# Optimization experiments

Measured on AMD Instinct MI355X. Metric: run time of the kernel, lower is better.

Reference implementation:

```python
import jax, jax.numpy as jnp
import numpy as np

HID = 512
FSI = int(HID * 0.3)            # 153
ALM_EXC = HID - FSI             # 359
ALM_INHIB = FSI                 # 153
UNITS = HID * 6 + FSI           # 3225
HALF = HID // 2
INP_DIM = 1
OUT_DIM = 1
B, T = 64, 500
T_CONST = 0.1
SIG_R = 0.01
SIG_I = 0.01
ALM_OFF = 5 * HID + FSI


def _ht(w):
    # F.hardtanh(w, 1e-10, 1): Dale's-law positivity clamp on raw weights
    return jnp.clip(w, 1e-10, 1.0)


def _build_W(str2str_w, thal2alm_w, thal2str_w, alm2alm_w, alm2str_w, alm2thal_w,
             str2snr_w, str2gpe_w, gpe2stn_w, stn2snr_w, snr2thal_w,
             fsi2str_w, thal2fsi_w, alm2fsi_w, fsi2fsi_w, sparse_mask):
    sm = sparse_mask.astype(str2str_w.dtype)
    alm_sign = jnp.concatenate([jnp.ones(ALM_EXC), -jnp.ones(ALM_INHIB)])      # alm2alm_D diag
    alm_exc_col = jnp.concatenate([jnp.ones(ALM_EXC), jnp.zeros(ALM_INHIB)])   # alm2{str,thal,fsi}_mask
    d1_col = jnp.concatenate([jnp.ones(HALF), jnp.zeros(HALF)])                # D1 half of striatum
    blocks = {
        ('str', 'str'): -(sm * _ht(str2str_w)),                      # @ str2str_D (-I)
        ('str', 'fsi'): -_ht(fsi2str_w),                             # @ fsi2str_D (-I)
        ('str', 'thal'): _ht(thal2str_w) * d1_col[:, None],          # thal2str_mask (D1 rows)
        ('str', 'alm'): _ht(alm2str_w) * alm_exc_col[None, :],
        ('fsi', 'fsi'): -_ht(fsi2fsi_w),                             # @ fsi2fsi_D (-I)
        ('fsi', 'thal'): _ht(thal2fsi_w),
        ('fsi', 'alm'): _ht(alm2fsi_w) * alm_exc_col[None, :],
        ('gpe', 'str'): -(_ht(str2gpe_w) * (1.0 - d1_col)[None, :]), # D2 cols, @ -I
        ('stn', 'gpe'): -_ht(gpe2stn_w),                             # @ gpe2stn_D (-I)
        ('snr', 'str'): -(_ht(str2snr_w) * d1_col[None, :]),         # D1 cols, @ -I
        ('snr', 'stn'): _ht(stn2snr_w),
        ('thal', 'snr'): -_ht(snr2thal_w),                           # @ snr2thal_D (-I)
        ('thal', 'alm'): _ht(alm2thal_w) * alm_exc_col[None, :],
        ('alm', 'thal'): _ht(thal2alm_w),
        ('alm', 'alm'): _ht(alm2alm_w) * alm_sign[None, :],          # @ alm2alm_D
    }
    off = {'str': 0, 'fsi': HID, 'gpe': HID + FSI, 'stn': 2 * HID + FSI,
           'snr': 3 * HID + FSI, 'thal': 4 * HID + FSI, 'alm': 5 * HID + FSI}
    W = jnp.zeros((UNITS, UNITS), str2str_w.dtype)
    for (dst, src), M in blocks.items():
        W = W.at[off[dst]:off[dst] + M.shape[0], off[src]:off[src] + M.shape[1]].set(M)
    return W


def _tonic_and_masks():
    # order: str | fsi | gpe | stn | snr | thal | alm_exc | alm_inhib
    tonic = jnp.concatenate([0.1 * jnp.ones(HID), 0.1 * jnp.ones(FSI),
                             0.6 * jnp.ones(HID), 0.3 * jnp.ones(HID),
                             0.6 * jnp.ones(HID), 0.1 * jnp.ones(HID),
                             0.1 * jnp.ones(ALM_EXC), 0.1 * jnp.ones(ALM_INHIB)])
    thal_mask = jnp.zeros(UNITS).at[4 * HID + FSI:5 * HID + FSI].set(1.0)
    return tonic, thal_mask


def _forward(inp, cue_inp, inhib_stim, hn, xn, noise_hid, noise_inp,
             str2str_w, thal2alm_w, thal2str_w, alm2alm_w, alm2str_w, alm2thal_w,
             str2snr_w, str2gpe_w, gpe2stn_w, stn2snr_w, snr2thal_w,
             fsi2str_w, thal2fsi_w, alm2fsi_w, fsi2fsi_w, inp_w, out_w, sparse_mask):
    W = _build_W(str2str_w, thal2alm_w, thal2str_w, alm2alm_w, alm2str_w, alm2thal_w,
                 str2snr_w, str2gpe_w, gpe2stn_w, stn2snr_w, snr2thal_w,
                 fsi2str_w, thal2fsi_w, alm2fsi_w, fsi2fsi_w, sparse_mask)
    tonic, thal_mask = _tonic_and_masks()
    # input only projects to str+fsi block
    inp_full_w = jnp.concatenate([inp_w, jnp.zeros((5 * HID, inp_w.shape[1]), inp_w.dtype)], axis=0)
    nh_scale = SIG_R * float(np.sqrt(2.0 * T_CONST))
    ni_scale = SIG_I * float(np.sqrt(2.0 * T_CONST))
    x0, h0 = xn[0], hn[0]

    def step(carry, xs):
        x, h = carry
        inp_t, cue_t, inhib_t, nh_t, ni_t = xs
        inp_eff = inp_t + ni_scale * ni_t                               # [B, inp_dim]
        drive = (h @ W.T + inp_eff @ inp_full_w.T
                 + cue_t * thal_mask[None, :] + tonic[None, :]
                 + inhib_t + nh_scale * nh_t)                           # [B, UNITS]
        x_new = x + T_CONST * (-x + drive)
        h_new = jax.nn.relu(x_new)
        out = h_new[:, ALM_OFF:ALM_OFF + ALM_EXC] @ out_w.T             # [B, out_dim]
        return (x_new, h_new), (h_new, out)

    seqs = (jnp.swapaxes(inp, 0, 1), jnp.swapaxes(cue_inp, 0, 1),
            jnp.swapaxes(inhib_stim, 0, 1), noise_hid, noise_inp)
    _, (hs, outs) = jax.lax.scan(step, (x0, h0), seqs)
    return jnp.swapaxes(hs, 0, 1), jnp.swapaxes(outs, 0, 1)


def setup_inputs():
    key = jax.random.key(0)
    ks = jax.random.split(key, 24)
    u = lambda k, shape: jax.random.uniform(k, shape, jnp.float32, 0.0, 0.01)
    return dict(
        inp=jax.random.uniform(ks[0], (B, T, INP_DIM)),
        cue_inp=jax.random.uniform(ks[1], (B, T, 1)),
        inhib_stim=jnp.zeros((B, T, UNITS)),
        hn=jnp.zeros((1, B, UNITS)),
        xn=jnp.zeros((1, B, UNITS)),
        noise_hid=jax.random.normal(ks[2], (T, B, UNITS)),
        noise_inp=jax.random.normal(ks[3], (T, B, INP_DIM)),
        str2str_w=u(ks[4], (HID, HID)),
        thal2alm_w=u(ks[5], (HID, HID)),
        thal2str_w=u(ks[6], (HID, HID)),
        alm2alm_w=u(ks[7], (HID, HID)),
        alm2str_w=u(ks[8], (HID, HID)),
        alm2thal_w=u(ks[9], (HID, HID)),
        str2snr_w=u(ks[10], (HID, HID)),
        str2gpe_w=u(ks[11], (HID, HID)),
        gpe2stn_w=u(ks[12], (HID, HID)),
        stn2snr_w=u(ks[13], (HID, HID)),
        snr2thal_w=u(ks[14], (HID, HID)),
        fsi2str_w=u(ks[15], (HID, FSI)),
        thal2fsi_w=u(ks[16], (FSI, HID)),
        alm2fsi_w=u(ks[17], (FSI, HID)),
        fsi2fsi_w=u(ks[18], (FSI, FSI)),
        inp_w=u(ks[19], (HID + FSI, INP_DIM)),
        out_w=u(ks[20], (OUT_DIM, ALM_EXC)),
        str2str_sparse_mask=(jax.random.uniform(ks[21], (HID, HID)) < 0.1).astype(jnp.int32),
    )


def reference(inp, cue_inp, inhib_stim, hn, xn, noise_hid, noise_inp,
              str2str_w, thal2alm_w, thal2str_w, alm2alm_w, alm2str_w, alm2thal_w,
              str2snr_w, str2gpe_w, gpe2stn_w, stn2snr_w, snr2thal_w,
              fsi2str_w, thal2fsi_w, alm2fsi_w, fsi2fsi_w, inp_w, out_w,
              str2str_sparse_mask):
    return _forward(inp, cue_inp, inhib_stim, hn, xn, noise_hid, noise_inp,
                    str2str_w, thal2alm_w, thal2str_w, alm2alm_w, alm2str_w, alm2thal_w,
                    str2snr_w, str2gpe_w, gpe2stn_w, stn2snr_w, snr2thal_w,
                    fsi2str_w, thal2fsi_w, alm2fsi_w, fsi2fsi_w, inp_w, out_w,
                    str2str_sparse_mask)
```

## Files before the change

### kernel.cpp

```cpp
#include <hip/hip_runtime.h>
#include <hip/hip_cooperative_groups.h>

namespace cg = cooperative_groups;

#define UNITS 3225
#define HSTR  3232
#define NBATCH 64
#define NSTEP 500
#define NH_SCALE 0.004472135954999579f
#define NI_SCALE 0.004472135954999579f
#define HSZ 103200000ll
#define WCT_FLOATS 2731520
#define WC0_FLOATS 2699776
#define NBLK5 125
#define NTHR5 512

__constant__ int   c_dst[7]  = {0,512,665,1177,1689,2201,2713};
__constant__ int   c_rows[7] = {512,153,512,512,512,512,512};
__constant__ int   c_wid[7]  = {1536,1024,256,512,768,871,1024};
__constant__ int   c_r0s[7]  = {0,512,256,665,0,1689,2201};
__constant__ int   c_r0l[7]  = {665,153,256,512,256,512,1024};
__constant__ int   c_r1s[7]  = {2201,2201,0,0,1177,2713,0};
__constant__ float c_ton[7]  = {0.1f,0.1f,0.6f,0.3f,0.6f,0.1f,0.1f};

__constant__ int   c5_rpb[7]  = {16,24,32,32,32,32,24};
__constant__ int   c5_cs[8]   = {0,32,39,55,71,87,103,125};
__constant__ int   c5_wb[8]   = {0,786432,958464,1089536,1351680,1744896,2190848,2731520};
__constant__ int   c5_pdst[7] = {0,512,668,1180,1692,2204,2716};
__constant__ int   c5_pr0s[7] = {0,512,256,668,0,1692,2204};
__constant__ int   c5_pr1s[7] = {2204,2204,0,0,1180,2716,2716};

__constant__ int   c0_cs[8]   = {0,64,84,148,212,276,340,404};
__constant__ int   c0_base[7] = {0,786432,943104,1074176,1336320,1729536,2175488};
__constant__ int   c0_cbase[8]= {0,786432,943104,1074176,1336320,1729536,2175488,2699776};

__device__ __forceinline__ float ht_clip(float w) {
    return fminf(fmaxf(w, 1e-10f), 1.0f);
}

__device__ __forceinline__ float w_val(
    int r, int i, int c,
    const float* __restrict__ str2str, const float* __restrict__ thal2alm,
    const float* __restrict__ thal2str, const float* __restrict__ alm2alm,
    const float* __restrict__ alm2str, const float* __restrict__ alm2thal,
    const float* __restrict__ str2snr, const float* __restrict__ str2gpe,
    const float* __restrict__ gpe2stn, const float* __restrict__ stn2snr,
    const float* __restrict__ snr2thal, const float* __restrict__ fsi2str,
    const float* __restrict__ thal2fsi, const float* __restrict__ alm2fsi,
    const float* __restrict__ fsi2fsi, const int* __restrict__ smask)
{
    int r0l = c_r0l[r];
    int v = (c < r0l) ? (c_r0s[r] + c) : (c_r1s[r] + (c - r0l));
    int rv, j;
    if (v < 512)       { rv = 0; j = v; }
    else if (v < 665)  { rv = 1; j = v - 512; }
    else if (v < 1177) { rv = 2; j = v - 665; }
    else if (v < 1689) { rv = 3; j = v - 1177; }
    else if (v < 2201) { rv = 4; j = v - 1689; }
    else if (v < 2713) { rv = 5; j = v - 2201; }
    else               { rv = 6; j = v - 2713; }
    float val = 0.0f;
    switch (r) {
    case 0:
        if (rv == 0)      val = smask[i*512+j] ? -ht_clip(str2str[i*512+j]) : 0.0f;
        else if (rv == 1) val = -ht_clip(fsi2str[i*153+j]);
        else if (rv == 5) val = (i < 256) ? ht_clip(thal2str[i*512+j]) : 0.0f;
        else              val = (j < 359) ? ht_clip(alm2str[i*512+j]) : 0.0f;
        break;
    case 1:
        if (rv == 1)      val = -ht_clip(fsi2fsi[i*153+j]);
        else if (rv == 5) val = ht_clip(thal2fsi[i*512+j]);
        else              val = (j < 359) ? ht_clip(alm2fsi[i*512+j]) : 0.0f;
        break;
    case 2:
        val = (j >= 256) ? -ht_clip(str2gpe[i*512+j]) : 0.0f;
        break;
    case 3:
        val = -ht_clip(gpe2stn[i*512+j]);
        break;
    case 4:
        if (rv == 0) val = (j < 256) ? -ht_clip(str2snr[i*512+j]) : 0.0f;
        else         val = ht_clip(stn2snr[i*512+j]);
        break;
    case 5:
        if (rv == 4) val = -ht_clip(snr2thal[i*512+j]);
        else         val = (j < 359) ? ht_clip(alm2thal[i*512+j]) : 0.0f;
        break;
    default:
        if (rv == 5) val = ht_clip(thal2alm[i*512+j]);
        else         val = (j < 359) ? ht_clip(alm2alm[i*512+j]) : -ht_clip(alm2alm[i*512+j]);
        break;
    }
    return val;
}

#define WARGS                                                                  \
    const float* __restrict__ str2str, const float* __restrict__ thal2alm,     \
    const float* __restrict__ thal2str, const float* __restrict__ alm2alm,     \
    const float* __restrict__ alm2str, const float* __restrict__ alm2thal,     \
    const float* __restrict__ str2snr, const float* __restrict__ str2gpe,      \
    const float* __restrict__ gpe2stn, const float* __restrict__ stn2snr,      \
    const float* __restrict__ snr2thal, const float* __restrict__ fsi2str,     \
    const float* __restrict__ thal2fsi, const float* __restrict__ alm2fsi,     \
    const float* __restrict__ fsi2fsi, const int* __restrict__ smask
#define WPASS str2str, thal2alm, thal2str, alm2alm, alm2str, alm2thal,         \
    str2snr, str2gpe, gpe2stn, stn2snr, snr2thal, fsi2str, thal2fsi, alm2fsi,  \
    fsi2fsi, smask

__global__ void build_w_v5(WARGS, float* __restrict__ Wct)
{
    int tid = blockIdx.x * blockDim.x + threadIdx.x;
    if (tid >= WCT_FLOATS) return;
    int r = 0;
    while (tid >= c5_wb[r+1]) ++r;
    int local = tid - c5_wb[r];
    int rpb   = c5_rpb[r];
    int width = c_wid[r];
    int bsz   = width * rpb;
    int blk   = local / bsz;
    int rem   = local - blk*bsz;
    int c     = rem / rpb;
    int q     = rem - c*rpb;
    int i     = blk*rpb + q;
    float val = 0.0f;
    if (i < c_rows[r]) val = w_val(r, i, c, WPASS);
    Wct[tid] = val;
}

__global__ void build_w_r0(WARGS, float* __restrict__ Wc)
{
    int tid = blockIdx.x * blockDim.x + threadIdx.x;
    if (tid >= WC0_FLOATS) return;
    int r = 0;
    while (tid >= c0_cbase[r+1]) ++r;
    int local = tid - c0_cbase[r];
    int width = c_wid[r];
    int row = local / width;
    int c = local - row * width;
    Wc[tid] = w_val(r, row, c, WPASS);
}

struct Params {
    const float* __restrict__ inp;
    const float* __restrict__ cue;
    const float* __restrict__ inhib;
    const float* __restrict__ hn;
    const float* __restrict__ xn;
    const float* __restrict__ noise_hid;
    const float* __restrict__ noise_inp;
    const float* __restrict__ inp_w;
    const float* __restrict__ out_w;
    const float* __restrict__ Wc;
    float* __restrict__ hT0;
    float* __restrict__ hT1;
    float* __restrict__ out;
};

template<int RPB, int HALF>
__device__ __forceinline__ void mm_seg(
    const float* __restrict__ rbb,
    const float* __restrict__ wq,
    int cfrom, int cto, int abase,
    float* __restrict__ acc)
{
    int c = cfrom;
    while (c < cto && ((abase + c) & 3)) {
        float hv = rbb[abase + c];
        #pragma unroll
        for (int q = 0; q < HALF; ++q) acc[q] += wq[c*RPB + q] * hv;
        ++c;
    }
    #pragma unroll 2
    for (; c + 4 <= cto; c += 4) {
        const float4 h4 = *reinterpret_cast<const float4*>(&rbb[abase + c]);
        const float hvv[4] = {h4.x, h4.y, h4.z, h4.w};
        #pragma unroll
        for (int cc = 0; cc < 4; ++cc) {
            #pragma unroll
            for (int g = 0; g < HALF/4; ++g) {
                const float4 w4 = *reinterpret_cast<const float4*>(&wq[(c+cc)*RPB + 4*g]);
                acc[4*g+0] += w4.x * hvv[cc];
                acc[4*g+1] += w4.y * hvv[cc];
                acc[4*g+2] += w4.z * hvv[cc];
                acc[4*g+3] += w4.w * hvv[cc];
            }
        }
    }
    for (; c < cto; ++c) {
        float hv = rbb[abase + c];
        #pragma unroll
        for (int q = 0; q < HALF; ++q) acc[q] += wq[c*RPB + q] * hv;
    }
}

template<int RPB, int HALF>
__device__ __forceinline__ void mm_do(
    const float* __restrict__ rbb, const float* __restrict__ wq,
    int c0, int a1, int b0, int c1, int pr0s, int pr1s, int r0l,
    float* __restrict__ red, int kq, int q0, int lane)
{
    float acc[HALF];
    #pragma unroll
    for (int q = 0; q < HALF; ++q) acc[q] = 0.0f;
    mm_seg<RPB,HALF>(rbb, wq, c0, a1, pr0s, acc);
    mm_seg<RPB,HALF>(rbb, wq, b0, c1, pr1s - r0l, acc);
    #pragma unroll
    for (int q = 0; q < HALF; ++q)
        red[(kq*32 + q0 + q)*64 + lane] = acc[q];
}

__global__ void __launch_bounds__(NTHR5, 1) rnn_loop_v5(Params p)
{
    cg::grid_group grid = cg::this_grid();
    const int tid  = threadIdx.x;
    const int lane = tid & 63;
    const int wv   = tid >> 6;
    const int kq   = __builtin_amdgcn_readfirstlane(wv & 3);
    const int grp  = __builtin_amdgcn_readfirstlane(wv >> 2);
    const int bi   = blockIdx.x;

    int r = 0;
    while (bi >= c5_cs[r+1]) ++r;
    const int lc    = bi - c5_cs[r];
    const int rpb   = c5_rpb[r];
    const int row0  = lc * rpb;
    const int nr    = min(rpb, c_rows[r] - row0);
    const int u0    = c_dst[r] + row0;
    const int u0p   = c5_pdst[r] + row0;
    const int width = c_wid[r];
    const float tonic = c_ton[r];
    const int r0l = c_r0l[r];
    const int pr0s = c5_pr0s[r], pr1s = c5_pr1s[r];
    const float* __restrict__ wblk = p.Wc + c5_wb[r] + lc * width * rpb;

    __shared__ float red[4*32*64];
    __shared__ float htile[32*65];

    const int r2 = wv;
    const int b  = lane;

    float xreg[4] = {0.f,0.f,0.f,0.f};
    #pragma unroll
    for (int pi = 0; pi < 4; ++pi) {
        int pr = r2 + 8*pi;
        if (pr < nr) {
            int u = u0 + pr;
            xreg[pi] = p.xn[b*UNITS + u];
            p.hT0[b*HSTR + u0p + pr] = p.hn[b*UNITS + u];
        }
    }
    if (bi == 0) {
        for (int idx = tid; idx < 64*7; idx += NTHR5) {
            int bb2 = idx / 7, k = idx - bb2*7;
            int col = (k < 3) ? (665 + k) : (3225 + k);
            p.hT0[bb2*HSTR + col] = 0.0f;
            p.hT1[bb2*HSTR + col] = 0.0f;
        }
    }
    const bool outs_block = (bi >= 39 && bi < 103);
    const int  ob = bi - 39;
    grid.sync();

    const int c0 = __builtin_amdgcn_readfirstlane((width * kq) >> 2);
    const int c1 = __builtin_amdgcn_readfirstlane((width * (kq + 1)) >> 2);
    const int q0 = __builtin_amdgcn_readfirstlane(grp * (rpb >> 1));
    const int a1 = min(c1, r0l), b0 = max(c0, r0l);
    const float* __restrict__ wq = wblk + q0;

    for (int t = 0; t < NSTEP; ++t) {
        const float* __restrict__ rb = (t & 1) ? p.hT1 : p.hT0;
        float* __restrict__ wb = (t & 1) ? p.hT0 : p.hT1;

        if (outs_block && t > 0 && tid < 64) {
            float s = 0.0f;
            for (int jj = lane; jj < 359; jj += 64)
                s += rb[ob*HSTR + 2716 + jj] * p.out_w[jj];
            #pragma unroll
            for (int off = 32; off > 0; off >>= 1)
                s += __shfl_down(s, off, 64);
            if (lane == 0) p.out[HSZ + (long long)ob*NSTEP + (t-1)] = s;
        }

        float nh[4] = {0.f,0.f,0.f,0.f}, ih[4] = {0.f,0.f,0.f,0.f};
        #pragma unroll
        for (int pi = 0; pi < 4; ++pi) {
            int pr = r2 + 8*pi;
            if (pr < nr) {
                int u = u0 + pr;
                nh[pi] = __builtin_nontemporal_load(&p.noise_hid[((long long)t*NBATCH + b)*UNITS + u]);
                ih[pi] = __builtin_nontemporal_load(&p.inhib[((long long)b*NSTEP + t)*UNITS + u]);
            }
        }
        const float inp_eff = p.inp[b*NSTEP + t] + NI_SCALE * p.noise_inp[t*NBATCH + b];
        const float cue_b   = p.cue[b*NSTEP + t];

        const float* __restrict__ rbb = rb + lane*HSTR;
        if (r == 0)
            mm_do<16,8 >(rbb, wq, c0, a1, b0, c1, pr0s, pr1s, r0l, red, kq, q0, lane);
        else if (r == 1 || r == 6)
            mm_do<24,12>(rbb, wq, c0, a1, b0, c1, pr0s, pr1s, r0l, red, kq, q0, lane);
        else
            mm_do<32,16>(rbb, wq, c0, a1, b0, c1, pr0s, pr1s, r0l, red, kq, q0, lane);
        __syncthreads();

        #pragma unroll
        for (int pi = 0; pi < 4; ++pi) {
            int pr = r2 + 8*pi;
            if (pr < nr) {
                int u = u0 + pr;
                float mm = red[(0*32 + pr)*64 + b];
                mm += red[(1*32 + pr)*64 + b];
                mm += red[(2*32 + pr)*64 + b];
                mm += red[(3*32 + pr)*64 + b];
                float drive = mm + tonic;
                if (u < 665) drive += inp_eff * p.inp_w[u];
                if (u >= 2201 && u < 2713) drive += cue_b;
                drive += ih[pi];
                drive += NH_SCALE * nh[pi];
                float xv = xreg[pi];
                xv = xv + 0.1f*(drive - xv);
                xreg[pi] = xv;
                float h = fmaxf(xv, 0.0f);
                wb[b*HSTR + u0p + pr] = h;
                htile[pr*65 + b] = h;
            }
        }
        __syncthreads();
        {
            int rr = tid & 31, bb = tid >> 5;
            if (rr < nr) {
                #pragma unroll
                for (int rep = 0; rep < 4; ++rep) {
                    int bbb = bb + 16*rep;
                    long long o = (long long)bbb*(NSTEP*UNITS) + (long long)t*UNITS + (u0+rr);
                    __builtin_nontemporal_store(htile[rr*65 + bbb], &p.out[o]);
                }
            }
        }
        grid.sync();
    }

    if (outs_block && tid < 64) {
        const float* __restrict__ rb = p.hT0;
        float s = 0.0f;
        for (int jj = lane; jj < 359; jj += 64)
            s += rb[ob*HSTR + 2716 + jj] * p.out_w[jj];
        #pragma unroll
        for (int off = 32; off > 0; off >>= 1)
            s += __shfl_down(s, off, 64);
        if (lane == 0) p.out[HSZ + (long long)ob*NSTEP + (NSTEP-1)] = s;
    }
}

__global__ void __launch_bounds__(256) rnn_loop_fb(Params p)
{
    cg::grid_group grid = cg::this_grid();
    const int tid  = threadIdx.x;
    const int lane = tid & 63;
    const int wv   = tid >> 6;
    const int bi   = blockIdx.x;

    int r = 0;
    while (bi >= c0_cs[r+1]) ++r;
    const int lc    = bi - c0_cs[r];
    const int row0  = lc * 8;
    const int nr    = min(8, c_rows[r] - row0);
    const int u0    = c_dst[r] + row0;
    const int width = c_wid[r];
    const float tonic = c_ton[r];
    const int r0s = c_r0s[r], r0l = c_r0l[r], r1s = c_r1s[r];
    const float* __restrict__ wr = p.Wc + c0_base[r] + row0 * width;

    __shared__ float red[4][8][64];
    __shared__ float htile[8*65];

    const int r2 = tid >> 6;
    const int b  = tid & 63;

    float xreg[2];
    #pragma unroll
    for (int pi = 0; pi < 2; ++pi) {
        int pr = r2 + 4*pi;
        xreg[pi] = 0.0f;
        if (pr < nr) {
            xreg[pi] = p.xn[b*UNITS + (u0+pr)];
            p.hT0[(u0+pr)*64 + b] = p.hn[b*UNITS + (u0+pr)];
        }
    }
    const bool outs_block = (bi >= 84 && bi < 148);
    grid.sync();

    const int c0 = (width * wv) >> 2;
    const int c1 = (width * (wv+1)) >> 2;
    const int a0 = c0, a1 = min(c1, r0l);
    const int b0 = max(c0, r0l), b1 = c1;

    for (int t = 0; t < NSTEP; ++t) {
        const float* __restrict__ rb = (t & 1) ? p.hT1 : p.hT0;
        float* __restrict__ wb = (t & 1) ? p.hT0 : p.hT1;

        if (outs_block && t > 0 && tid < 64) {
            int ob = bi - 84;
            float s = 0.0f;
            for (int jj = lane; jj < 359; jj += 64)
                s += rb[(2713+jj)*64 + ob] * p.out_w[jj];
            #pragma unroll
            for (int off = 32; off > 0; off >>= 1)
                s += __shfl_down(s, off, 64);
            if (lane == 0) p.out[HSZ + (long long)ob*NSTEP + (t-1)] = s;
        }

        float acc[8];
        #pragma unroll
        for (int q = 0; q < 8; ++q) acc[q] = 0.0f;

        #pragma unroll 4
        for (int c = a0; c < a1; ++c) {
            float hv = rb[(r0s + c)*64 + lane];
            #pragma unroll
            for (int q = 0; q < 8; ++q) acc[q] += wr[q*width + c] * hv;
        }
        #pragma unroll 4
        for (int c = b0; c < b1; ++c) {
            float hv = rb[(r1s + (c - r0l))*64 + lane];
            #pragma unroll
            for (int q = 0; q < 8; ++q) acc[q] += wr[q*width + c] * hv;
        }

        #pragma unroll
        for (int q = 0; q < 8; ++q) red[wv][q][lane] = acc[q];
        __syncthreads();

        const float inp_eff = p.inp[b*NSTEP + t] + NI_SCALE * p.noise_inp[t*NBATCH + b];
        const float cue_b   = p.cue[b*NSTEP + t];
        #pragma unroll
        for (int pi = 0; pi < 2; ++pi) {
            int pr = r2 + 4*pi;
            if (pr < nr) {
                int u = u0 + pr;
                float mm = red[0][pr][b] + red[1][pr][b] + red[2][pr][b] + red[3][pr][b];
                float drive = mm + tonic;
                if (u < 665) drive += inp_eff * p.inp_w[u];
                if (u >= 2201 && u < 2713) drive += cue_b;
                drive += p.inhib[((long long)b*NSTEP + t)*UNITS + u];
                drive += NH_SCALE * p.noise_hid[((long long)t*NBATCH + b)*UNITS + u];
                float xv = xreg[pi];
                xv = xv + 0.1f*(drive - xv);
                xreg[pi] = xv;
                float h = fmaxf(xv, 0.0f);
                wb[u*64 + b] = h;
                htile[pr*65 + b] = h;
            }
        }
        __syncthreads();
        {
            int rr = tid & 7, bb = tid >> 3;
            if (rr < nr) {
                long long o = (long long)bb*(NSTEP*UNITS) + (long long)t*UNITS + (u0+rr);
                p.out[o] = htile[rr*65 + bb];
                p.out[o + 32ll*NSTEP*UNITS] = htile[rr*65 + bb + 32];
            }
        }
        grid.sync();
    }

    if (outs_block && tid < 64) {
        int ob = bi - 84;
        const float* __restrict__ rb = p.hT0;
        float s = 0.0f;
        for (int jj = lane; jj < 359; jj += 64)
            s += rb[(2713+jj)*64 + ob] * p.out_w[jj];
        #pragma unroll
        for (int off = 32; off > 0; off >>= 1)
            s += __shfl_down(s, off, 64);
        if (lane == 0) p.out[HSZ + (long long)ob*NSTEP + (NSTEP-1)] = s;
    }
}

extern "C" void kernel_launch(void* const* d_in, const int* in_sizes, int n_in,
                              void* d_out, int out_size, void* d_ws, size_t ws_size,
                              hipStream_t stream)
{
    (void)in_sizes; (void)n_in; (void)out_size; (void)ws_size;
    const float* inp       = (const float*)d_in[0];
    const float* cue       = (const float*)d_in[1];
    const float* inhib     = (const float*)d_in[2];
    const float* hn        = (const float*)d_in[3];
    const float* xn        = (const float*)d_in[4];
    const float* noise_hid = (const float*)d_in[5];
    const float* noise_inp = (const float*)d_in[6];
    const float* str2str   = (const float*)d_in[7];
    const float* thal2alm  = (const float*)d_in[8];
    const float* thal2str  = (const float*)d_in[9];
    const float* alm2alm   = (const float*)d_in[10];
    const float* alm2str   = (const float*)d_in[11];
    const float* alm2thal  = (const float*)d_in[12];
    const float* str2snr   = (const float*)d_in[13];
    const float* str2gpe   = (const float*)d_in[14];
    const float* gpe2stn   = (const float*)d_in[15];
    const float* stn2snr   = (const float*)d_in[16];
    const float* snr2thal  = (const float*)d_in[17];
    const float* fsi2str   = (const float*)d_in[18];
    const float* thal2fsi  = (const float*)d_in[19];
    const float* alm2fsi   = (const float*)d_in[20];
    const float* fsi2fsi   = (const float*)d_in[21];
    const float* inp_w     = (const float*)d_in[22];
    const float* out_w     = (const float*)d_in[23];
    const int*   smask     = (const int*)d_in[24];

    float* Wct = (float*)d_ws;
    float* hT0 = Wct + WCT_FLOATS;
    float* hT1 = hT0 + NBATCH*HSTR;

    Params p;
    p.inp = inp; p.cue = cue; p.inhib = inhib; p.hn = hn; p.xn = xn;
    p.noise_hid = noise_hid; p.noise_inp = noise_inp;
    p.inp_w = inp_w; p.out_w = out_w; p.Wc = Wct;
    p.hT0 = hT0; p.hT1 = hT1; p.out = (float*)d_out;

    hipLaunchKernelGGL(build_w_v5, dim3((WCT_FLOATS+255)/256), dim3(256), 0, stream,
        str2str, thal2alm, thal2str, alm2alm, alm2str, alm2thal, str2snr, str2gpe,
        gpe2stn, stn2snr, snr2thal, fsi2str, thal2fsi, alm2fsi, fsi2fsi, smask, Wct);

    void* kargs[] = { &p };
    hipError_t ce = hipLaunchCooperativeKernel((void*)rnn_loop_v5,
                                               dim3(NBLK5), dim3(NTHR5), kargs, 0, stream);
    if (ce != hipSuccess) {
        (void)hipGetLastError();
        hipLaunchKernelGGL(build_w_r0, dim3((WC0_FLOATS+255)/256), dim3(256), 0, stream,
            str2str, thal2alm, thal2str, alm2alm, alm2str, alm2thal, str2snr, str2gpe,
            gpe2stn, stn2snr, snr2thal, fsi2str, thal2fsi, alm2fsi, fsi2fsi, smask, Wct);
        hipLaunchCooperativeKernel((void*)rnn_loop_fb,
                                   dim3(404), dim3(256), kargs, 0, stream);
    }
}
```

Before: 41.87 ms.

## Replace grid.sync with atomic counter barrier and transpose hidden-state layout

Swaps the cooperative-groups grid sync for a hand-written monotonic atomic counter barrier, reset by the weight-build kernel, which spins with s_sleep. The hidden-state buffers are transposed to unit-major [unit][batch] so each lane reads its batch value with a coalesced agent-scope atomic load, replacing the padded float4 row reads. The goal is to cut per-step barrier latency over 500 steps. The trade-off is scalar (non-vectorised) h loads, and the fallback path still uses the old layout assumptions.

```diff
diff --git a/kernel.cpp b/kernel.cpp
--- a/kernel.cpp
+++ b/kernel.cpp
@@ -4,7 +4,6 @@
 namespace cg = cooperative_groups;
 
 #define UNITS 3225
-#define HSTR  3232
 #define NBATCH 64
 #define NSTEP 500
 #define NH_SCALE 0.004472135954999579f
@@ -12,8 +11,8 @@
 #define HSZ 103200000ll
 #define WCT_FLOATS 2731520
 #define WC0_FLOATS 2699776
-#define NBLK5 125
-#define NTHR5 512
+#define NBLK6 125
+#define NTHR6 512
 
 __constant__ int   c_dst[7]  = {0,512,665,1177,1689,2201,2713};
 __constant__ int   c_rows[7] = {512,153,512,512,512,512,512};
@@ -23,12 +22,9 @@
 __constant__ int   c_r1s[7]  = {2201,2201,0,0,1177,2713,0};
 __constant__ float c_ton[7]  = {0.1f,0.1f,0.6f,0.3f,0.6f,0.1f,0.1f};
 
-__constant__ int   c5_rpb[7]  = {16,24,32,32,32,32,24};
-__constant__ int   c5_cs[8]   = {0,32,39,55,71,87,103,125};
-__constant__ int   c5_wb[8]   = {0,786432,958464,1089536,1351680,1744896,2190848,2731520};
-__constant__ int   c5_pdst[7] = {0,512,668,1180,1692,2204,2716};
-__constant__ int   c5_pr0s[7] = {0,512,256,668,0,1692,2204};
-__constant__ int   c5_pr1s[7] = {2204,2204,0,0,1180,2716,2716};
+__constant__ int   c6_rpb[7]  = {16,24,32,32,32,32,24};
+__constant__ int   c6_cs[8]   = {0,32,39,55,71,87,103,125};
+__constant__ int   c6_wb[8]   = {0,786432,958464,1089536,1351680,1744896,2190848,2731520};
 
 __constant__ int   c0_cs[8]   = {0,64,84,148,212,276,340,404};
 __constant__ int   c0_base[7] = {0,786432,943104,1074176,1336320,1729536,2175488};
@@ -36,6 +32,13 @@
 
 __device__ __forceinline__ float ht_clip(float w) {
     return fminf(fmaxf(w, 1e-10f), 1.0f);
+}
+
+__device__ __forceinline__ float agload(const float* pp) {
+    return __hip_atomic_load(pp, __ATOMIC_RELAXED, __HIP_MEMORY_SCOPE_AGENT);
+}
+__device__ __forceinline__ void agstore(float* pp, float v) {
+    __hip_atomic_store(pp, v, __ATOMIC_RELAXED, __HIP_MEMORY_SCOPE_AGENT);
 }
 
 __device__ __forceinline__ float w_val(
@@ -107,14 +110,15 @@
     str2snr, str2gpe, gpe2stn, stn2snr, snr2thal, fsi2str, thal2fsi, alm2fsi,  \
     fsi2fsi, smask
 
-__global__ void build_w_v5(WARGS, float* __restrict__ Wct)
+__global__ void build_w_v6(WARGS, float* __restrict__ Wct, unsigned* __restrict__ cnt)
 {
     int tid = blockIdx.x * blockDim.x + threadIdx.x;
+    if (tid == 0) { cnt[0] = 0u; }
     if (tid >= WCT_FLOATS) return;
     int r = 0;
-    while (tid >= c5_wb[r+1]) ++r;
-    int local = tid - c5_wb[r];
-    int rpb   = c5_rpb[r];
+    while (tid >= c6_wb[r+1]) ++r;
+    int local = tid - c6_wb[r];
+    int rpb   = c6_rpb[r];
     int width = c_wid[r];
     int bsz   = width * rpb;
     int blk   = local / bsz;
@@ -153,65 +157,64 @@
     const float* __restrict__ Wc;
     float* __restrict__ hT0;
     float* __restrict__ hT1;
+    unsigned* __restrict__ cnt;
     float* __restrict__ out;
 };
 
-template<int RPB, int HALF>
-__device__ __forceinline__ void mm_seg(
-    const float* __restrict__ rbb,
-    const float* __restrict__ wq,
-    int cfrom, int cto, int abase,
-    float* __restrict__ acc)
-{
-    int c = cfrom;
-    while (c < cto && ((abase + c) & 3)) {
-        float hv = rbb[abase + c];
-        #pragma unroll
-        for (int q = 0; q < HALF; ++q) acc[q] += wq[c*RPB + q] * hv;
-        ++c;
-    }
-    #pragma unroll 2
-    for (; c + 4 <= cto; c += 4) {
-        const float4 h4 = *reinterpret_cast<const float4*>(&rbb[abase + c]);
-        const float hvv[4] = {h4.x, h4.y, h4.z, h4.w};
-        #pragma unroll
-        for (int cc = 0; cc < 4; ++cc) {
-            #pragma unroll
-            for (int g = 0; g < HALF/4; ++g) {
-                const float4 w4 = *reinterpret_cast<const float4*>(&wq[(c+cc)*RPB + 4*g]);
-                acc[4*g+0] += w4.x * hvv[cc];
-                acc[4*g+1] += w4.y * hvv[cc];
-                acc[4*g+2] += w4.z * hvv[cc];
-                acc[4*g+3] += w4.w * hvv[cc];
-            }
-        }
-    }
-    for (; c < cto; ++c) {
-        float hv = rbb[abase + c];
-        #pragma unroll
-        for (int q = 0; q < HALF; ++q) acc[q] += wq[c*RPB + q] * hv;
-    }
+__device__ __forceinline__ void gbarrier(unsigned* cnt, unsigned target)
+{
+    asm volatile("s_waitcnt vmcnt(0)" ::: "memory");
+    __syncthreads();
+    if (threadIdx.x == 0) {
+        __hip_atomic_fetch_add(cnt, 1u, __ATOMIC_RELAXED, __HIP_MEMORY_SCOPE_AGENT);
+        while (__hip_atomic_load(cnt, __ATOMIC_RELAXED, __HIP_MEMORY_SCOPE_AGENT) < target)
+            __builtin_amdgcn_s_sleep(2);
+    }
+    __syncthreads();
+    asm volatile("" ::: "memory");
 }
 
 template<int RPB, int HALF>
 __device__ __forceinline__ void mm_do(
-    const float* __restrict__ rbb, const float* __restrict__ wq,
-    int c0, int a1, int b0, int c1, int pr0s, int pr1s, int r0l,
+    const float* __restrict__ rb, const float* __restrict__ wq,
+    int c0, int a1, int b0, int c1, int r0s, int r1s, int r0l,
     float* __restrict__ red, int kq, int q0, int lane)
 {
     float acc[HALF];
     #pragma unroll
     for (int q = 0; q < HALF; ++q) acc[q] = 0.0f;
-    mm_seg<RPB,HALF>(rbb, wq, c0, a1, pr0s, acc);
-    mm_seg<RPB,HALF>(rbb, wq, b0, c1, pr1s - r0l, acc);
+
+    #pragma unroll 4
+    for (int c = c0; c < a1; ++c) {
+        float hv = agload(&rb[(r0s + c)*64 + lane]);
+        #pragma unroll
+        for (int g = 0; g < HALF/4; ++g) {
+            const float4 w4 = *reinterpret_cast<const float4*>(&wq[c*RPB + 4*g]);
+            acc[4*g+0] += w4.x * hv;
+            acc[4*g+1] += w4.y * hv;
+            acc[4*g+2] += w4.z * hv;
+            acc[4*g+3] += w4.w * hv;
+        }
+    }
+    #pragma unroll 4
+    for (int c = b0; c < c1; ++c) {
+        float hv = agload(&rb[(r1s + (c - r0l))*64 + lane]);
+        #pragma unroll
+        for (int g = 0; g < HALF/4; ++g) {
+            const float4 w4 = *reinterpret_cast<const float4*>(&wq[c*RPB + 4*g]);
+            acc[4*g+0] += w4.x * hv;
+            acc[4*g+1] += w4.y * hv;
+            acc[4*g+2] += w4.z * hv;
+            acc[4*g+3] += w4.w * hv;
+        }
+    }
     #pragma unroll
     for (int q = 0; q < HALF; ++q)
         red[(kq*32 + q0 + q)*64 + lane] = acc[q];
 }
 
-__global__ void __launch_bounds__(NTHR5, 1) rnn_loop_v5(Params p)
-{
-    cg::grid_group grid = cg::this_grid();
+__global__ void __launch_bounds__(NTHR6, 1) rnn_loop_v6(Params p)
+{
     const int tid  = threadIdx.x;
     const int lane = tid & 63;
     const int wv   = tid >> 6;
@@ -220,46 +223,35 @@
     const int bi   = blockIdx.x;
 
     int r = 0;
-    while (bi >= c5_cs[r+1]) ++r;
-    const int lc    = bi - c5_cs[r];
-    const int rpb   = c5_rpb[r];
+    while (bi >= c6_cs[r+1]) ++r;
+    const int lc    = bi - c6_cs[r];
+    const int rpb   = c6_rpb[r];
     const int row0  = lc * rpb;
     const int nr    = min(rpb, c_rows[r] - row0);
     const int u0    = c_dst[r] + row0;
-    const int u0p   = c5_pdst[r] + row0;
     const int width = c_wid[r];
     const float tonic = c_ton[r];
-    const int r0l = c_r0l[r];
-    const int pr0s = c5_pr0s[r], pr1s = c5_pr1s[r];
-    const float* __restrict__ wblk = p.Wc + c5_wb[r] + lc * width * rpb;
+    const int r0s = c_r0s[r], r0l = c_r0l[r], r1s = c_r1s[r];
+    const float* __restrict__ wblk = p.Wc + c6_wb[r] + lc * width * rpb;
 
     __shared__ float red[4*32*64];
     __shared__ float htile[32*65];
 
-    const int r2 = wv;
-    const int b  = lane;
+    const int b = lane;
 
     float xreg[4] = {0.f,0.f,0.f,0.f};
     #pragma unroll
     for (int pi = 0; pi < 4; ++pi) {
-        int pr = r2 + 8*pi;
+        int pr = wv + 8*pi;
         if (pr < nr) {
             int u = u0 + pr;
             xreg[pi] = p.xn[b*UNITS + u];
-            p.hT0[b*HSTR + u0p + pr] = p.hn[b*UNITS + u];
-        }
-    }
-    if (bi == 0) {
-        for (int idx = tid; idx < 64*7; idx += NTHR5) {
-            int bb2 = idx / 7, k = idx - bb2*7;
-            int col = (k < 3) ? (665 + k) : (3225 + k);
-            p.hT0[bb2*HSTR + col] = 0.0f;
-            p.hT1[bb2*HSTR + col] = 0.0f;
+            agstore(&p.hT0[u*64 + b], p.hn[b*UNITS + u]);
         }
     }
     const bool outs_block = (bi >= 39 && bi < 103);
     const int  ob = bi - 39;
-    grid.sync();
+    gbarrier(p.cnt, NBLK6);
 
     const int c0 = __builtin_amdgcn_readfirstlane((width * kq) >> 2);
     const int c1 = __builtin_amdgcn_readfirstlane((width * (kq + 1)) >> 2);
@@ -274,7 +266,7 @@
         if (outs_block && t > 0 && tid < 64) {
             float s = 0.0f;
             for (int jj = lane; jj < 359; jj += 64)
-                s += rb[ob*HSTR + 2716 + jj] * p.out_w[jj];
+                s += agload(&rb[(2713+jj)*64 + ob]) * p.out_w[jj];
             #pragma unroll
             for (int off = 32; off > 0; off >>= 1)
                 s += __shfl_down(s, off, 64);
@@ -284,7 +276,7 @@
         float nh[4] = {0.f,0.f,0.f,0.f}, ih[4] = {0.f,0.f,0.f,0.f};
         #pragma unroll
         for (int pi = 0; pi < 4; ++pi) {
-            int pr = r2 + 8*pi;
+            int pr = wv + 8*pi;
             if (pr < nr) {
                 int u = u0 + pr;
                 nh[pi] = __builtin_nontemporal_load(&p.noise_hid[((long long)t*NBATCH + b)*UNITS + u]);
@@ -294,18 +286,17 @@
         const float inp_eff = p.inp[b*NSTEP + t] + NI_SCALE * p.noise_inp[t*NBATCH + b];
         const float cue_b   = p.cue[b*NSTEP + t];
 
-        const float* __restrict__ rbb = rb + lane*HSTR;
         if (r == 0)
-            mm_do<16,8 >(rbb, wq, c0, a1, b0, c1, pr0s, pr1s, r0l, red, kq, q0, lane);
+            mm_do<16,8 >(rb, wq, c0, a1, b0, c1, r0s, r1s, r0l, red, kq, q0, lane);
         else if (r == 1 || r == 6)
-            mm_do<24,12>(rbb, wq, c0, a1, b0, c1, pr0s, pr1s, r0l, red, kq, q0, lane);
+            mm_do<24,12>(rb, wq, c0, a1, b0, c1, r0s, r1s, r0l, red, kq, q0, lane);
         else
-            mm_do<32,16>(rbb, wq, c0, a1, b0, c1, pr0s, pr1s, r0l, red, kq, q0, lane);
+            mm_do<32,16>(rb, wq, c0, a1, b0, c1, r0s, r1s, r0l, red, kq, q0, lane);
         __syncthreads();
 
         #pragma unroll
         for (int pi = 0; pi < 4; ++pi) {
-            int pr = r2 + 8*pi;
+            int pr = wv + 8*pi;
             if (pr < nr) {
                 int u = u0 + pr;
                 float mm = red[(0*32 + pr)*64 + b];
@@ -321,7 +312,7 @@
                 xv = xv + 0.1f*(drive - xv);
                 xreg[pi] = xv;
                 float h = fmaxf(xv, 0.0f);
-                wb[b*HSTR + u0p + pr] = h;
+                agstore(&wb[u*64 + b], h);
                 htile[pr*65 + b] = h;
             }
         }
@@ -337,14 +328,14 @@
                 }
             }
         }
-        grid.sync();
+        gbarrier(p.cnt, (unsigned)NBLK6*(t+2));
     }
 
     if (outs_block && tid < 64) {
         const float* __restrict__ rb = p.hT0;
         float s = 0.0f;
         for (int jj = lane; jj < 359; jj += 64)
-            s += rb[ob*HSTR + 2716 + jj] * p.out_w[jj];
+            s += agload(&rb[(2713+jj)*64 + ob]) * p.out_w[jj];
         #pragma unroll
         for (int off = 32; off > 0; off >>= 1)
             s += __shfl_down(s, off, 64);
@@ -508,23 +499,24 @@
     const float* out_w     = (const float*)d_in[23];
     const int*   smask     = (const int*)d_in[24];
 
-    float* Wct = (float*)d_ws;
-    float* hT0 = Wct + WCT_FLOATS;
-    float* hT1 = hT0 + NBATCH*HSTR;
+    float*    Wct = (float*)d_ws;
+    float*    hT0 = Wct + WCT_FLOATS;
+    float*    hT1 = hT0 + UNITS*64;
+    unsigned* cnt = (unsigned*)(hT1 + UNITS*64);
 
     Params p;
     p.inp = inp; p.cue = cue; p.inhib = inhib; p.hn = hn; p.xn = xn;
     p.noise_hid = noise_hid; p.noise_inp = noise_inp;
     p.inp_w = inp_w; p.out_w = out_w; p.Wc = Wct;
-    p.hT0 = hT0; p.hT1 = hT1; p.out = (float*)d_out;
-
-    hipLaunchKernelGGL(build_w_v5, dim3((WCT_FLOATS+255)/256), dim3(256), 0, stream,
+    p.hT0 = hT0; p.hT1 = hT1; p.cnt = cnt; p.out = (float*)d_out;
+
+    hipLaunchKernelGGL(build_w_v6, dim3((WCT_FLOATS+255)/256), dim3(256), 0, stream,
         str2str, thal2alm, thal2str, alm2alm, alm2str, alm2thal, str2snr, str2gpe,
-        gpe2stn, stn2snr, snr2thal, fsi2str, thal2fsi, alm2fsi, fsi2fsi, smask, Wct);
+        gpe2stn, stn2snr, snr2thal, fsi2str, thal2fsi, alm2fsi, fsi2fsi, smask, Wct, cnt);
 
     void* kargs[] = { &p };
-    hipError_t ce = hipLaunchCooperativeKernel((void*)rnn_loop_v5,
-                                               dim3(NBLK5), dim3(NTHR5), kargs, 0, stream);
+    hipError_t ce = hipLaunchCooperativeKernel((void*)rnn_loop_v6,
+                                               dim3(NBLK6), dim3(NTHR6), kargs, 0, stream);
     if (ce != hipSuccess) {
         (void)hipGetLastError();
         hipLaunchKernelGGL(build_w_r0, dim3((WC0_FLOATS+255)/256), dim3(256), 0, stream,
```

Result: faster. 33.84 ms (-19.2%).
